# Kernel optimization log

Measured on AMD Instinct MI355X. Metric: run time of the kernel, lower is better.

Reference implementation:

```python
import jax, jax.numpy as jnp
import numpy as np

B, S, D, DM, H, DH, DF, L, T = 4096, 64, 256, 512, 4, 64, 512, 6, 20


def mish(x):
    return x * jnp.tanh(jax.nn.softplus(x))


def layernorm(x, eps=1e-5):
    mu = jnp.mean(x, axis=-1, keepdims=True)
    var = jnp.var(x, axis=-1, keepdims=True)
    return (x - mu) * jax.lax.rsqrt(var + eps)


def setup_inputs() -> dict:
    key = jax.random.key(0)
    ks = iter(jax.random.split(key, 32))
    w = lambda *shape: jax.random.normal(next(ks), shape, dtype=jnp.float32) * 0.02
    inp = {
        'x_t': jax.random.normal(next(ks), (B, S, D), dtype=jnp.float32),
        't': jax.random.randint(next(ks), (B,), 0, T + 1),
        'backbone_latent': jax.random.normal(next(ks), (B, S, DM), dtype=jnp.float32),
        # timestep embedding
        'emb': w(T + 1, D),
        'te_w1': w(D, 4 * D), 'te_b1': jnp.zeros((4 * D,), jnp.float32),
        'te_w2': w(4 * D, D), 'te_b2': jnp.zeros((D,), jnp.float32),
        # cond projection
        'cp_w1': w(DM, D), 'cp_b1': jnp.zeros((D,), jnp.float32),
        'cp_w2': w(D, D), 'cp_b2': jnp.zeros((D,), jnp.float32),
        # stacked per-layer DiT block params [L, ...]
        'adaln_w': w(L, D, 6 * D), 'adaln_b': jnp.zeros((L, 6 * D), jnp.float32),
        'qkv_w': w(L, D, 3 * D), 'qkv_b': jnp.zeros((L, 3 * D), jnp.float32),
        'op_w': w(L, D, D), 'op_b': jnp.zeros((L, D), jnp.float32),
        'ffn_w1': w(L, D, DF), 'ffn_b1': jnp.zeros((L, DF), jnp.float32),
        'ffn_w2': w(L, DF, D), 'ffn_b2': jnp.zeros((L, D), jnp.float32),
        # final adaLN + projection (random here for nontrivial test, zero-init in original)
        'fa_w': w(D, 2 * D), 'fa_b': jnp.zeros((2 * D,), jnp.float32),
        'fp_w': w(D, D), 'fp_b': jnp.zeros((D,), jnp.float32),
    }
    return inp


def _forward(x_t, t, backbone_latent, emb, te_w1, te_b1, te_w2, te_b2,
             cp_w1, cp_b1, cp_w2, cp_b2, adaln_w, adaln_b, qkv_w, qkv_b,
             op_w, op_b, ffn_w1, ffn_b1, ffn_w2, ffn_b2, fa_w, fa_b, fp_w, fp_b):
    # conditioning vector c: [B, D]
    te = emb[t]                                   # [B, D]
    te = mish(te @ te_w1 + te_b1) @ te_w2 + te_b2
    cond = jnp.mean(backbone_latent, axis=1)      # [B, DM]
    cond = mish(cond @ cp_w1 + cp_b1) @ cp_w2 + cp_b2
    c = te + cond
    mc = mish(c)

    x = x_t
    for l in range(L):
        mod = (mc @ adaln_w[l] + adaln_b[l])[:, None, :]   # [B, 1, 6D]
        sh1, sc1, g1, sh2, sc2, g2 = jnp.split(mod, 6, axis=-1)
        # attention sub-block
        h = layernorm(x) * (1.0 + sc1) + sh1
        qkv = (h @ qkv_w[l] + qkv_b[l]).reshape(B, S, 3, H, DH)
        q = qkv[:, :, 0].transpose(0, 2, 1, 3)   # [B, H, S, DH]
        k = qkv[:, :, 1].transpose(0, 2, 1, 3)
        v = qkv[:, :, 2].transpose(0, 2, 1, 3)
        attn = jax.nn.softmax(jnp.einsum('bhsd,bhtd->bhst', q, k) * DH ** -0.5, axis=-1)
        h = jnp.einsum('bhst,bhtd->bhsd', attn, v).transpose(0, 2, 1, 3).reshape(B, S, D)
        h = h @ op_w[l] + op_b[l]
        x = x + g1 * h
        # FFN sub-block
        h = layernorm(x) * (1.0 + sc2) + sh2
        h = mish(h @ ffn_w1[l] + ffn_b1[l]) @ ffn_w2[l] + ffn_b2[l]
        x = x + g2 * h

    mod = (mc @ fa_w + fa_b)[:, None, :]
    shift, scale = jnp.split(mod, 2, axis=-1)
    x = layernorm(x) * (1.0 + scale) + shift
    return x @ fp_w + fp_b


def reference(x_t, t, backbone_latent, emb, te_w1, te_b1, te_w2, te_b2,
              cp_w1, cp_b1, cp_w2, cp_b2, adaln_w, adaln_b, qkv_w, qkv_b,
              op_w, op_b, ffn_w1, ffn_b1, ffn_w2, ffn_b2, fa_w, fa_b, fp_w, fp_b):
    return _forward(x_t, t, backbone_latent, emb, te_w1, te_b1, te_w2, te_b2,
                    cp_w1, cp_b1, cp_w2, cp_b2, adaln_w, adaln_b, qkv_w, qkv_b,
                    op_w, op_b, ffn_w1, ffn_b1, ffn_w2, ffn_b2, fa_w, fa_b, fp_w, fp_b)
```

## Files before the change

### kernel.cpp

```cpp
#include <hip/hip_runtime.h>

typedef unsigned short u16;
typedef float f32x4 __attribute__((ext_vector_type(4)));
typedef __bf16 bf16x8 __attribute__((ext_vector_type(8)));

__device__ __forceinline__ u16 f2b(float f) {
  unsigned u = __builtin_bit_cast(unsigned, f);
  u += 0x7FFF + ((u >> 16) & 1);
  return (u16)(u >> 16);
}

__device__ __forceinline__ float mishf(float x) {
  float e = __expf(fminf(x, 20.f));
  float n = e * (e + 2.f);
  return x * __fdividef(n, n + 2.f);
}

__device__ __forceinline__ void gl_lds16(const void* g, void* l) {
  __builtin_amdgcn_global_load_lds((__attribute__((address_space(1))) void*)g,
                                   (__attribute__((address_space(3))) void*)l, 16, 0, 0);
}

__device__ __forceinline__ bf16x8 ldb8(const u16* p) {
  return __builtin_bit_cast(bf16x8, *(const uint4*)p);
}

__global__ __launch_bounds__(256)
void transpose_w(const float* __restrict__ in, u16* __restrict__ out, int K, int N) {
  __shared__ float tl[64][65];
  const long zoff = (long)blockIdx.z * K * N;
  in += zoff; out += zoff;
  const int n0 = blockIdx.x * 64, k0 = blockIdx.y * 64;
  const int c = threadIdx.x & 63, r0 = threadIdx.x >> 6;
#pragma unroll
  for (int i = 0; i < 16; ++i) {
    int r = i * 4 + r0;
    tl[r][c] = in[(long)(k0 + r) * N + n0 + c];
  }
  __syncthreads();
#pragma unroll
  for (int i = 0; i < 16; ++i) {
    int r = i * 4 + r0;
    out[(long)(n0 + r) * K + k0 + c] = f2b(tl[c][r]);
  }
}

__global__ __launch_bounds__(1024)
void te_table_kernel(const float* __restrict__ emb, const float* __restrict__ w1,
                     const float* __restrict__ b1, const float* __restrict__ w2,
                     const float* __restrict__ b2, float* __restrict__ table) {
  __shared__ float te[256];
  __shared__ float h1[1024];
  __shared__ float red[1024];
  const int tt = blockIdx.x, tid = threadIdx.x;
  if (tid < 256) te[tid] = emb[tt * 256 + tid];
  __syncthreads();
  float a = b1[tid];
#pragma unroll 8
  for (int k = 0; k < 256; ++k) a += te[k] * w1[k * 1024 + tid];
  h1[tid] = mishf(a);
  __syncthreads();
  const int j = tid & 255, kq = tid >> 8;
  float a2 = 0.f;
#pragma unroll 8
  for (int k = kq * 256; k < kq * 256 + 256; ++k) a2 += h1[k] * w2[k * 256 + j];
  red[tid] = a2;
  __syncthreads();
  if (tid < 256)
    table[tt * 256 + tid] = b2[tid] + red[tid] + red[tid + 256] + red[tid + 512] + red[tid + 768];
}

__global__ __launch_bounds__(256)
void cond_mean_kernel(const float* __restrict__ bb, u16* __restrict__ cond) {
  const int b = blockIdx.x, tid = threadIdx.x;
  const float* p = bb + (long)b * 64 * 512;
  for (int d = tid; d < 512; d += 256) {
    float s = 0.f;
#pragma unroll
    for (int t = 0; t < 64; ++t) s += p[t * 512 + d];
    cond[b * 512 + d] = f2b(s * (1.f / 64.f));
  }
}

__global__ __launch_bounds__(256)
void ln_mod(const float* __restrict__ x, const float* __restrict__ modb,
            int mstride, int shoff, int scoff, u16* __restrict__ out) {
  const int lane = threadIdx.x & 63;
  const long row = (long)blockIdx.x * 4 + (threadIdx.x >> 6);
  const float4 xv = *(const float4*)(x + row * 256 + lane * 4);
  float s1 = xv.x + xv.y + xv.z + xv.w;
  float s2 = xv.x * xv.x + xv.y * xv.y + xv.z * xv.z + xv.w * xv.w;
#pragma unroll
  for (int m = 1; m < 64; m <<= 1) { s1 += __shfl_xor(s1, m); s2 += __shfl_xor(s2, m); }
  const float mean = s1 * (1.f / 256.f);
  float var = s2 * (1.f / 256.f) - mean * mean;
  const float rstd = rsqrtf(fmaxf(var, 0.f) + 1e-5f);
  const long b = row >> 6;
  const float4 sc = *(const float4*)(modb + b * mstride + scoff + lane * 4);
  const float4 sh = *(const float4*)(modb + b * mstride + shoff + lane * 4);
  ushort4 o;
  o.x = f2b((xv.x - mean) * rstd * (1.f + sc.x) + sh.x);
  o.y = f2b((xv.y - mean) * rstd * (1.f + sc.y) + sh.y);
  o.z = f2b((xv.z - mean) * rstd * (1.f + sc.z) + sh.z);
  o.w = f2b((xv.w - mean) * rstd * (1.f + sc.w) + sh.w);
  *(ushort4*)(out + row * 256 + lane * 4) = o;
}

template <int EPI>
__global__ __launch_bounds__(256)
void gemm_bt(const u16* __restrict__ A, const u16* __restrict__ Bt,
             const float* __restrict__ bias, void* __restrict__ outp,
             const int* __restrict__ tvec, const float* __restrict__ tetab,
             int M, int N, int K) {
  __shared__ __align__(16) u16 As[2][128 * 64];
  __shared__ __align__(16) u16 Bs[2][128 * 64];
  const int tid = threadIdx.x;
  const int lane = tid & 63;
  const int wave = tid >> 6;
  const int wr = (wave >> 1) << 6;
  const int wc = (wave & 1) << 6;
  const long tm = (long)blockIdx.y * 128;
  const long tn = (long)blockIdx.x * 128;
  const u16* Ag = A + tm * K;
  const u16* Bg = Bt + tn * K;
  f32x4 acc[4][4] = {};
  const int kcb = lane >> 4;
  const int swz = lane & 7;
  const int NT = K >> 6;

  auto stage = [&](int t, int buf) {
    const int k0 = t << 6;
#pragma unroll
    for (int i = 0; i < 4; ++i) {
      int c = tid + (i << 8);
      int r = c >> 3;
      int sch = (c & 7) ^ (r & 7);
      gl_lds16(Ag + (long)r * K + k0 + (sch << 3), &As[buf][c << 3]);
    }
#pragma unroll
    for (int i = 0; i < 4; ++i) {
      int c = tid + (i << 8);
      int r = c >> 3;
      int sch = (c & 7) ^ (r & 7);
      gl_lds16(Bg + (long)r * K + k0 + (sch << 3), &Bs[buf][c << 3]);
    }
  };

  stage(0, 0);
  __syncthreads();
  int cur = 0;
  for (int t = 0; t < NT; ++t) {
    if (t + 1 < NT) stage(t + 1, cur ^ 1);
#pragma unroll
    for (int kt = 0; kt < 2; ++kt) {
      const int ko = ((kt * 4 + kcb) ^ swz) << 3;
      bf16x8 av[4], bv[4];
#pragma unroll
      for (int mt = 0; mt < 4; ++mt)
        av[mt] = ldb8(&As[cur][(wr + mt * 16 + (lane & 15)) * 64 + ko]);
#pragma unroll
      for (int nt = 0; nt < 4; ++nt)
        bv[nt] = ldb8(&Bs[cur][(wc + nt * 16 + (lane & 15)) * 64 + ko]);
#pragma unroll
      for (int mt = 0; mt < 4; ++mt)
#pragma unroll
        for (int nt = 0; nt < 4; ++nt)
          acc[mt][nt] = __builtin_amdgcn_mfma_f32_16x16x32_bf16(bv[nt], av[mt], acc[mt][nt], 0, 0, 0);
    }
    __syncthreads();
    cur ^= 1;
  }
  const int rl = lane & 15;
  const int c4 = (lane >> 4) << 2;
  f32x4 b4[4];
#pragma unroll
  for (int nt = 0; nt < 4; ++nt)
    b4[nt] = *(const f32x4*)(bias + (int)tn + wc + nt * 16 + c4);
#pragma unroll
  for (int mt = 0; mt < 4; ++mt) {
    const unsigned row = (unsigned)(tm + wr + mt * 16 + rl);
    const unsigned rb = row * (unsigned)N;
#pragma unroll
    for (int nt = 0; nt < 4; ++nt) {
      const unsigned col = (unsigned)tn + wc + nt * 16 + c4;
      f32x4 v = acc[mt][nt] + b4[nt];
      if constexpr (EPI == 0) {
        ushort4 o;
        o.x = f2b(v[0]); o.y = f2b(v[1]); o.z = f2b(v[2]); o.w = f2b(v[3]);
        *(ushort4*)((u16*)outp + rb + col) = o;
      } else if constexpr (EPI == 1) {
        ushort4 o;
        o.x = f2b(mishf(v[0])); o.y = f2b(mishf(v[1]));
        o.z = f2b(mishf(v[2])); o.w = f2b(mishf(v[3]));
        *(ushort4*)((u16*)outp + rb + col) = o;
      } else if constexpr (EPI == 3) {
        *(f32x4*)((float*)outp + rb + col) = v;
      } else {
        const f32x4 te = *(const f32x4*)(tetab + tvec[row] * 256 + col);
        ushort4 o;
        o.x = f2b(mishf(v[0] + te[0])); o.y = f2b(mishf(v[1] + te[1]));
        o.z = f2b(mishf(v[2] + te[2])); o.w = f2b(mishf(v[3] + te[3]));
        *(ushort4*)((u16*)outp + rb + col) = o;
      }
    }
  }
}

__global__ __launch_bounds__(256)
void gemm_ln(const u16* __restrict__ A, const u16* __restrict__ Bt,
             const float* __restrict__ bias, const float* __restrict__ xin,
             const float* __restrict__ gptr,
             const float* __restrict__ lnsh, const float* __restrict__ lnsc, int lnstride,
             float* __restrict__ xout, u16* __restrict__ hout, int K) {
  __shared__ __align__(16) u16 As[2][64 * 64];
  __shared__ __align__(16) u16 Bs[2][256 * 64];
  const int tid = threadIdx.x, lane = tid & 63, wave = tid >> 6;
  const int wr = wave * 16;
  const long tm = (long)blockIdx.x * 64;
  const u16* Ag = A + tm * K;
  f32x4 acc[16] = {};
  const int kcb = lane >> 4, swz = lane & 7;
  const int NT = K >> 6;

  auto stage = [&](int t, int buf) {
    const int k0 = t << 6;
#pragma unroll
    for (int i = 0; i < 2; ++i) {
      int c = tid + (i << 8);
      int r = c >> 3;
      int sch = (c & 7) ^ (r & 7);
      gl_lds16(Ag + (long)r * K + k0 + (sch << 3), &As[buf][c << 3]);
    }
#pragma unroll
    for (int i = 0; i < 8; ++i) {
      int c = tid + (i << 8);
      int r = c >> 3;
      int sch = (c & 7) ^ (r & 7);
      gl_lds16(Bt + (long)r * K + k0 + (sch << 3), &Bs[buf][c << 3]);
    }
  };

  stage(0, 0);
  __syncthreads();
  int cur = 0;
  for (int t = 0; t < NT; ++t) {
    if (t + 1 < NT) stage(t + 1, cur ^ 1);
#pragma unroll
    for (int kt = 0; kt < 2; ++kt) {
      const int ko = ((kt * 4 + kcb) ^ swz) << 3;
      bf16x8 av = ldb8(&As[cur][(wr + (lane & 15)) * 64 + ko]);
#pragma unroll
      for (int nt = 0; nt < 16; ++nt) {
        bf16x8 bv = ldb8(&Bs[cur][(nt * 16 + (lane & 15)) * 64 + ko]);
        acc[nt] = __builtin_amdgcn_mfma_f32_16x16x32_bf16(bv, av, acc[nt], 0, 0, 0);
      }
    }
    __syncthreads();
    cur ^= 1;
  }
  const int rl = lane & 15;
  const int c4 = (lane >> 4) << 2;
  const long row = tm + wr + rl;
  const long b = blockIdx.x;
  float s1 = 0.f, s2 = 0.f;
#pragma unroll
  for (int nt = 0; nt < 16; ++nt) {
    const int col = nt * 16 + c4;
    const f32x4 b4 = *(const f32x4*)(bias + col);
    const f32x4 g4 = *(const f32x4*)(gptr + b * 1536 + col);
    const f32x4 x = *(const f32x4*)(xin + row * 256 + col);
    f32x4 xn = x + g4 * (acc[nt] + b4);
    acc[nt] = xn;
    s1 += xn[0] + xn[1] + xn[2] + xn[3];
    s2 += xn[0] * xn[0] + xn[1] * xn[1] + xn[2] * xn[2] + xn[3] * xn[3];
  }
  s1 += __shfl_xor(s1, 16); s1 += __shfl_xor(s1, 32);
  s2 += __shfl_xor(s2, 16); s2 += __shfl_xor(s2, 32);
  const float mean = s1 * (1.f / 256.f);
  const float var = s2 * (1.f / 256.f) - mean * mean;
  const float rstd = rsqrtf(fmaxf(var, 0.f) + 1e-5f);
#pragma unroll
  for (int nt = 0; nt < 16; ++nt) {
    const int col = nt * 16 + c4;
    const f32x4 sc4 = *(const f32x4*)(lnsc + b * lnstride + col);
    const f32x4 sh4 = *(const f32x4*)(lnsh + b * lnstride + col);
    *(f32x4*)(xout + row * 256 + col) = acc[nt];
    f32x4 h = (acc[nt] - mean) * rstd * (1.f + sc4) + sh4;
    ushort4 o;
    o.x = f2b(h[0]); o.y = f2b(h[1]); o.z = f2b(h[2]); o.w = f2b(h[3]);
    *(ushort4*)(hout + row * 256 + col) = o;
  }
}

__global__ __launch_bounds__(128)
void attn_kernel(const u16* __restrict__ qkv, u16* __restrict__ out) {
  __shared__ __align__(16) u16 vt_s[2][64 * 72];
  __shared__ __align__(16) u16 p_s[2][64 * 72];
  const int lane = threadIdx.x & 63;
  const int wave = threadIdx.x >> 6;
  const long b = blockIdx.x >> 1;
  const int h = ((blockIdx.x & 1) << 1) | wave;
  u16* vt = vt_s[wave];
  u16* pl = p_s[wave];
  const u16* base = qkv + b * (64 * 768);
#pragma unroll
  for (int it = 0; it < 8; ++it) {
    int chunk = it * 64 + lane;
    int t = chunk >> 3, dhb = (chunk & 7) << 3;
    union { uint4 u; u16 s[8]; } uv;
    uv.u = *(const uint4*)(base + t * 768 + 512 + h * 64 + dhb);
#pragma unroll
    for (int j = 0; j < 8; ++j) vt[(dhb + j) * 72 + t] = uv.s[j];
  }
  const u16* qb = base + h * 64;
  const u16* kb = base + 256 + h * 64;
  f32x4 sacc[4][4] = {};
#pragma unroll
  for (int kt = 0; kt < 2; ++kt) {
    bf16x8 qa[4], kv[4];
#pragma unroll
    for (int mt = 0; mt < 4; ++mt)
      qa[mt] = ldb8(qb + ((lane & 15) + mt * 16) * 768 + kt * 32 + ((lane >> 4) << 3));
#pragma unroll
    for (int nt = 0; nt < 4; ++nt)
      kv[nt] = ldb8(kb + ((lane & 15) + nt * 16) * 768 + kt * 32 + ((lane >> 4) << 3));
#pragma unroll
    for (int mt = 0; mt < 4; ++mt)
#pragma unroll
      for (int nt = 0; nt < 4; ++nt)
        sacc[mt][nt] = __builtin_amdgcn_mfma_f32_16x16x32_bf16(qa[mt], kv[nt], sacc[mt][nt], 0, 0, 0);
  }
  const float scale = 0.125f;
#pragma unroll
  for (int mt = 0; mt < 4; ++mt) {
#pragma unroll
    for (int r = 0; r < 4; ++r) {
      float mx = fmaxf(fmaxf(sacc[mt][0][r], sacc[mt][1][r]), fmaxf(sacc[mt][2][r], sacc[mt][3][r]));
#pragma unroll
      for (int m = 1; m <= 8; m <<= 1) mx = fmaxf(mx, __shfl_xor(mx, m));
      float p[4];
      float sum = 0.f;
#pragma unroll
      for (int nt = 0; nt < 4; ++nt) { p[nt] = __expf((sacc[mt][nt][r] - mx) * scale); sum += p[nt]; }
#pragma unroll
      for (int m = 1; m <= 8; m <<= 1) sum += __shfl_xor(sum, m);
      const float rinv = 1.f / sum;
      const int s = mt * 16 + ((lane >> 4) << 2) + r;
#pragma unroll
      for (int nt = 0; nt < 4; ++nt) pl[s * 72 + nt * 16 + (lane & 15)] = f2b(p[nt] * rinv);
    }
  }
  __syncthreads();
  f32x4 oacc[4][4] = {};
#pragma unroll
  for (int kt = 0; kt < 2; ++kt) {
    bf16x8 pa[4], vv[4];
#pragma unroll
    for (int mt = 0; mt < 4; ++mt)
      pa[mt] = ldb8(pl + ((lane & 15) + mt * 16) * 72 + kt * 32 + ((lane >> 4) << 3));
#pragma unroll
    for (int nt = 0; nt < 4; ++nt)
      vv[nt] = ldb8(vt + ((lane & 15) + nt * 16) * 72 + kt * 32 + ((lane >> 4) << 3));
#pragma unroll
    for (int mt = 0; mt < 4; ++mt)
#pragma unroll
      for (int nt = 0; nt < 4; ++nt)
        oacc[mt][nt] = __builtin_amdgcn_mfma_f32_16x16x32_bf16(vv[nt], pa[mt], oacc[mt][nt], 0, 0, 0);
  }
  u16* ob = out + b * (64 * 256) + h * 64;
#pragma unroll
  for (int mt = 0; mt < 4; ++mt)
#pragma unroll
    for (int nt = 0; nt < 4; ++nt) {
      const int s = mt * 16 + (lane & 15);
      const int d4 = nt * 16 + ((lane >> 4) << 2);
      ushort4 o;
      o.x = f2b(oacc[mt][nt][0]); o.y = f2b(oacc[mt][nt][1]);
      o.z = f2b(oacc[mt][nt][2]); o.w = f2b(oacc[mt][nt][3]);
      *(ushort4*)(ob + s * 256 + d4) = o;
    }
}

extern "C" void kernel_launch(void* const* d_in, const int* in_sizes, int n_in,
                              void* d_out, int out_size, void* d_ws, size_t ws_size,
                              hipStream_t stream) {
  (void)in_sizes; (void)n_in; (void)out_size; (void)ws_size;
  const int B = 4096, L = 6;
  const long BSr = (long)B * 64;

  const float* x_t = (const float*)d_in[0];
  const int* tvec = (const int*)d_in[1];
  const float* backbone = (const float*)d_in[2];
  const float* emb = (const float*)d_in[3];
  const float* te_w1 = (const float*)d_in[4];
  const float* te_b1 = (const float*)d_in[5];
  const float* te_w2 = (const float*)d_in[6];
  const float* te_b2 = (const float*)d_in[7];
  const float* cp_w1 = (const float*)d_in[8];
  const float* cp_b1 = (const float*)d_in[9];
  const float* cp_w2 = (const float*)d_in[10];
  const float* cp_b2 = (const float*)d_in[11];
  const float* adaln_w = (const float*)d_in[12];
  const float* adaln_b = (const float*)d_in[13];
  const float* qkv_w = (const float*)d_in[14];
  const float* qkv_b = (const float*)d_in[15];
  const float* op_w = (const float*)d_in[16];
  const float* op_b = (const float*)d_in[17];
  const float* ffn_w1 = (const float*)d_in[18];
  const float* ffn_b1 = (const float*)d_in[19];
  const float* ffn_w2 = (const float*)d_in[20];
  const float* ffn_b2 = (const float*)d_in[21];
  const float* fa_w = (const float*)d_in[22];
  const float* fa_b = (const float*)d_in[23];
  const float* fp_w = (const float*)d_in[24];
  const float* fp_b = (const float*)d_in[25];

  char* w = (char*)d_ws;
  auto alloc = [&](size_t bytes) { char* p = w; w += (bytes + 255) & ~(size_t)255; return p; };
  u16* WT_cp1 = (u16*)alloc(256L * 512 * 2);
  u16* WT_cp2 = (u16*)alloc(256L * 256 * 2);
  u16* WT_adaln = (u16*)alloc(6L * 1536 * 256 * 2);
  u16* WT_qkv = (u16*)alloc(6L * 768 * 256 * 2);
  u16* WT_op = (u16*)alloc(6L * 256 * 256 * 2);
  u16* WT_f1 = (u16*)alloc(6L * 512 * 256 * 2);
  u16* WT_f2 = (u16*)alloc(6L * 256 * 512 * 2);
  u16* WT_fa = (u16*)alloc(512L * 256 * 2);
  u16* WT_fp = (u16*)alloc(256L * 256 * 2);
  float* te_tab = (float*)alloc(21L * 256 * 4);
  u16* cond = (u16*)alloc(4096L * 512 * 2);
  u16* c1 = (u16*)alloc(4096L * 256 * 2);
  u16* mc = (u16*)alloc(4096L * 256 * 2);
  float* modb6 = (float*)alloc(6L * 4096 * 1536 * 4);
  float* famod = (float*)alloc(4096L * 512 * 4);
  u16* hbuf = (u16*)alloc(BSr * 256 * 2);
  u16* qkvbuf = (u16*)alloc(BSr * 768 * 2);
  float* xbuf = (float*)d_out;

  transpose_w<<<dim3(4, 8, 1), 256, 0, stream>>>(cp_w1, WT_cp1, 512, 256);
  transpose_w<<<dim3(4, 4, 1), 256, 0, stream>>>(cp_w2, WT_cp2, 256, 256);
  transpose_w<<<dim3(24, 4, 6), 256, 0, stream>>>(adaln_w, WT_adaln, 256, 1536);
  transpose_w<<<dim3(12, 4, 6), 256, 0, stream>>>(qkv_w, WT_qkv, 256, 768);
  transpose_w<<<dim3(4, 4, 6), 256, 0, stream>>>(op_w, WT_op, 256, 256);
  transpose_w<<<dim3(8, 4, 6), 256, 0, stream>>>(ffn_w1, WT_f1, 256, 512);
  transpose_w<<<dim3(4, 8, 6), 256, 0, stream>>>(ffn_w2, WT_f2, 512, 256);
  transpose_w<<<dim3(8, 4, 1), 256, 0, stream>>>(fa_w, WT_fa, 256, 512);
  transpose_w<<<dim3(4, 4, 1), 256, 0, stream>>>(fp_w, WT_fp, 256, 256);

  te_table_kernel<<<21, 1024, 0, stream>>>(emb, te_w1, te_b1, te_w2, te_b2, te_tab);
  cond_mean_kernel<<<4096, 256, 0, stream>>>(backbone, cond);

  gemm_bt<1><<<dim3(2, 32), 256, 0, stream>>>(cond, WT_cp1, cp_b1, c1, nullptr, nullptr, 4096, 256, 512);
  gemm_bt<4><<<dim3(2, 32), 256, 0, stream>>>(c1, WT_cp2, cp_b2, mc, tvec, te_tab, 4096, 256, 256);
  gemm_bt<3><<<dim3(4, 32), 256, 0, stream>>>(mc, WT_fa, fa_b, famod, nullptr, nullptr, 4096, 512, 256);
  for (int l = 0; l < L; ++l)
    gemm_bt<3><<<dim3(12, 32), 256, 0, stream>>>(mc, WT_adaln + (long)l * 1536 * 256, adaln_b + l * 1536,
                                                 modb6 + (long)l * 4096 * 1536, nullptr, nullptr, 4096, 1536, 256);

  ln_mod<<<BSr / 4, 256, 0, stream>>>(x_t, modb6, 1536, 0, 256, hbuf);

  for (int l = 0; l < L; ++l) {
    const float* mb = modb6 + (long)l * 4096 * 1536;
    gemm_bt<0><<<dim3(6, BSr / 128), 256, 0, stream>>>(hbuf, WT_qkv + (long)l * 768 * 256, qkv_b + l * 768,
                                                       qkvbuf, nullptr, nullptr, (int)BSr, 768, 256);
    attn_kernel<<<B * 2, 128, 0, stream>>>(qkvbuf, hbuf);
    gemm_ln<<<BSr / 64, 256, 0, stream>>>(hbuf, WT_op + (long)l * 256 * 256, op_b + l * 256,
                                          (l == 0) ? x_t : xbuf, mb + 512,
                                          mb + 768, mb + 1024, 1536, xbuf, hbuf, 256);
    gemm_bt<1><<<dim3(4, BSr / 128), 256, 0, stream>>>(hbuf, WT_f1 + (long)l * 512 * 256, ffn_b1 + l * 512,
                                                       qkvbuf, nullptr, nullptr, (int)BSr, 512, 256);
    const float* nsh = (l < 5) ? (modb6 + (long)(l + 1) * 4096 * 1536) : famod;
    const float* nsc = (l < 5) ? (modb6 + (long)(l + 1) * 4096 * 1536 + 256) : (famod + 256);
    const int nstride = (l < 5) ? 1536 : 512;
    gemm_ln<<<BSr / 64, 256, 0, stream>>>(qkvbuf, WT_f2 + (long)l * 256 * 512, ffn_b2 + l * 256,
                                          xbuf, mb + 1280, nsh, nsc, nstride, xbuf, hbuf, 512);
  }
  gemm_bt<3><<<dim3(2, BSr / 128), 256, 0, stream>>>(hbuf, WT_fp, fp_b, d_out, nullptr, nullptr, (int)BSr, 256, 256);
}
```

Measured before the change: 7.059 ms.

## Retile gemm_ln waves to 64x64 subtiles with cross-wave LayerNorm reduction

Each wave in the fused GEMM+residual+LayerNorm kernel now computes a 64-row by 64-column subtile instead of 16 rows by all 256 columns. This cuts the shared-memory B-fragment reads per MFMA, since each wave now loads 4 A and 4 B fragments for 16 MFMAs instead of 1 A and 16 B. Because a row is now split across waves, row sums go through shared memory with an extra barrier. The residual, gate and bias loads are also issued before the main loop so they overlap the first stage, and K becomes a template parameter. The prefetched values raise register pressure.

```diff
diff --git a/kernel.cpp b/kernel.cpp
--- a/kernel.cpp
+++ b/kernel.cpp
@@ -206,20 +206,22 @@
   }
 }
 
+template <int K>
 __global__ __launch_bounds__(256)
 void gemm_ln(const u16* __restrict__ A, const u16* __restrict__ Bt,
              const float* __restrict__ bias, const float* __restrict__ xin,
              const float* __restrict__ gptr,
              const float* __restrict__ lnsh, const float* __restrict__ lnsc, int lnstride,
-             float* __restrict__ xout, u16* __restrict__ hout, int K) {
+             float* __restrict__ xout, u16* __restrict__ hout) {
   __shared__ __align__(16) u16 As[2][64 * 64];
   __shared__ __align__(16) u16 Bs[2][256 * 64];
   const int tid = threadIdx.x, lane = tid & 63, wave = tid >> 6;
-  const int wr = wave * 16;
+  const int wc = wave << 6;
   const long tm = (long)blockIdx.x * 64;
   const u16* Ag = A + tm * K;
-  f32x4 acc[16] = {};
-  const int kcb = lane >> 4, swz = lane & 7;
+  const int rl = lane & 15;
+  const int c4 = (lane >> 4) << 2;
+  const int swz = lane & 7;
   const int NT = K >> 6;
 
   auto stage = [&](int t, int buf) {
@@ -241,54 +243,94 @@
   };
 
   stage(0, 0);
-  __syncthreads();
+  const long b = blockIdx.x;
+  f32x4 xr[4][4], g4[4], b4[4];
+#pragma unroll
+  for (int nt = 0; nt < 4; ++nt) {
+    const int col = wc + nt * 16 + c4;
+    b4[nt] = *(const f32x4*)(bias + col);
+    g4[nt] = *(const f32x4*)(gptr + b * 1536 + col);
+#pragma unroll
+    for (int mt = 0; mt < 4; ++mt)
+      xr[mt][nt] = *(const f32x4*)(xin + (tm + mt * 16 + rl) * 256 + col);
+  }
+  __syncthreads();
+
+  f32x4 acc[4][4] = {};
   int cur = 0;
   for (int t = 0; t < NT; ++t) {
     if (t + 1 < NT) stage(t + 1, cur ^ 1);
 #pragma unroll
     for (int kt = 0; kt < 2; ++kt) {
-      const int ko = ((kt * 4 + kcb) ^ swz) << 3;
-      bf16x8 av = ldb8(&As[cur][(wr + (lane & 15)) * 64 + ko]);
-#pragma unroll
-      for (int nt = 0; nt < 16; ++nt) {
-        bf16x8 bv = ldb8(&Bs[cur][(nt * 16 + (lane & 15)) * 64 + ko]);
-        acc[nt] = __builtin_amdgcn_mfma_f32_16x16x32_bf16(bv, av, acc[nt], 0, 0, 0);
-      }
+      const int ko = ((kt * 4 + (lane >> 4)) ^ swz) << 3;
+      bf16x8 av[4], bv[4];
+#pragma unroll
+      for (int mt = 0; mt < 4; ++mt)
+        av[mt] = ldb8(&As[cur][(mt * 16 + rl) * 64 + ko]);
+#pragma unroll
+      for (int nt = 0; nt < 4; ++nt)
+        bv[nt] = ldb8(&Bs[cur][(wc + nt * 16 + rl) * 64 + ko]);
+#pragma unroll
+      for (int mt = 0; mt < 4; ++mt)
+#pragma unroll
+        for (int nt = 0; nt < 4; ++nt)
+          acc[mt][nt] = __builtin_amdgcn_mfma_f32_16x16x32_bf16(bv[nt], av[mt], acc[mt][nt], 0, 0, 0);
     }
     __syncthreads();
     cur ^= 1;
   }
-  const int rl = lane & 15;
-  const int c4 = (lane >> 4) << 2;
-  const long row = tm + wr + rl;
-  const long b = blockIdx.x;
-  float s1 = 0.f, s2 = 0.f;
-#pragma unroll
-  for (int nt = 0; nt < 16; ++nt) {
-    const int col = nt * 16 + c4;
-    const f32x4 b4 = *(const f32x4*)(bias + col);
-    const f32x4 g4 = *(const f32x4*)(gptr + b * 1536 + col);
-    const f32x4 x = *(const f32x4*)(xin + row * 256 + col);
-    f32x4 xn = x + g4 * (acc[nt] + b4);
-    acc[nt] = xn;
-    s1 += xn[0] + xn[1] + xn[2] + xn[3];
-    s2 += xn[0] * xn[0] + xn[1] * xn[1] + xn[2] * xn[2] + xn[3] * xn[3];
-  }
-  s1 += __shfl_xor(s1, 16); s1 += __shfl_xor(s1, 32);
-  s2 += __shfl_xor(s2, 16); s2 += __shfl_xor(s2, 32);
-  const float mean = s1 * (1.f / 256.f);
-  const float var = s2 * (1.f / 256.f) - mean * mean;
-  const float rstd = rsqrtf(fmaxf(var, 0.f) + 1e-5f);
-#pragma unroll
-  for (int nt = 0; nt < 16; ++nt) {
-    const int col = nt * 16 + c4;
+
+  float s1[4] = {}, s2[4] = {};
+#pragma unroll
+  for (int mt = 0; mt < 4; ++mt)
+#pragma unroll
+    for (int nt = 0; nt < 4; ++nt) {
+      f32x4 xn = xr[mt][nt] + g4[nt] * (acc[mt][nt] + b4[nt]);
+      acc[mt][nt] = xn;
+      s1[mt] += xn[0] + xn[1] + xn[2] + xn[3];
+      s2[mt] += xn[0] * xn[0] + xn[1] * xn[1] + xn[2] * xn[2] + xn[3] * xn[3];
+    }
+#pragma unroll
+  for (int mt = 0; mt < 4; ++mt) {
+    s1[mt] += __shfl_xor(s1[mt], 16); s1[mt] += __shfl_xor(s1[mt], 32);
+    s2[mt] += __shfl_xor(s2[mt], 16); s2[mt] += __shfl_xor(s2[mt], 32);
+  }
+  float* st = (float*)&As[0][0];
+  if (lane < 16) {
+#pragma unroll
+    for (int mt = 0; mt < 4; ++mt) {
+      st[wave * 128 + mt * 16 + lane] = s1[mt];
+      st[wave * 128 + 64 + mt * 16 + lane] = s2[mt];
+    }
+  }
+  __syncthreads();
+  float mean[4], rstd[4];
+#pragma unroll
+  for (int mt = 0; mt < 4; ++mt) {
+    float a = 0.f, q = 0.f;
+#pragma unroll
+    for (int w2 = 0; w2 < 4; ++w2) {
+      a += st[w2 * 128 + mt * 16 + rl];
+      q += st[w2 * 128 + 64 + mt * 16 + rl];
+    }
+    mean[mt] = a * (1.f / 256.f);
+    float var = q * (1.f / 256.f) - mean[mt] * mean[mt];
+    rstd[mt] = rsqrtf(fmaxf(var, 0.f) + 1e-5f);
+  }
+#pragma unroll
+  for (int nt = 0; nt < 4; ++nt) {
+    const int col = wc + nt * 16 + c4;
     const f32x4 sc4 = *(const f32x4*)(lnsc + b * lnstride + col);
     const f32x4 sh4 = *(const f32x4*)(lnsh + b * lnstride + col);
-    *(f32x4*)(xout + row * 256 + col) = acc[nt];
-    f32x4 h = (acc[nt] - mean) * rstd * (1.f + sc4) + sh4;
-    ushort4 o;
-    o.x = f2b(h[0]); o.y = f2b(h[1]); o.z = f2b(h[2]); o.w = f2b(h[3]);
-    *(ushort4*)(hout + row * 256 + col) = o;
+#pragma unroll
+    for (int mt = 0; mt < 4; ++mt) {
+      const long row = tm + mt * 16 + rl;
+      *(f32x4*)(xout + row * 256 + col) = acc[mt][nt];
+      f32x4 h = (acc[mt][nt] - mean[mt]) * rstd[mt] * (1.f + sc4) + sh4;
+      ushort4 o;
+      o.x = f2b(h[0]); o.y = f2b(h[1]); o.z = f2b(h[2]); o.w = f2b(h[3]);
+      *(ushort4*)(hout + row * 256 + col) = o;
+    }
   }
 }
 
@@ -463,16 +505,16 @@
     gemm_bt<0><<<dim3(6, BSr / 128), 256, 0, stream>>>(hbuf, WT_qkv + (long)l * 768 * 256, qkv_b + l * 768,
                                                        qkvbuf, nullptr, nullptr, (int)BSr, 768, 256);
     attn_kernel<<<B * 2, 128, 0, stream>>>(qkvbuf, hbuf);
-    gemm_ln<<<BSr / 64, 256, 0, stream>>>(hbuf, WT_op + (long)l * 256 * 256, op_b + l * 256,
-                                          (l == 0) ? x_t : xbuf, mb + 512,
-                                          mb + 768, mb + 1024, 1536, xbuf, hbuf, 256);
+    gemm_ln<256><<<BSr / 64, 256, 0, stream>>>(hbuf, WT_op + (long)l * 256 * 256, op_b + l * 256,
+                                               (l == 0) ? x_t : xbuf, mb + 512,
+                                               mb + 768, mb + 1024, 1536, xbuf, hbuf);
     gemm_bt<1><<<dim3(4, BSr / 128), 256, 0, stream>>>(hbuf, WT_f1 + (long)l * 512 * 256, ffn_b1 + l * 512,
                                                        qkvbuf, nullptr, nullptr, (int)BSr, 512, 256);
     const float* nsh = (l < 5) ? (modb6 + (long)(l + 1) * 4096 * 1536) : famod;
     const float* nsc = (l < 5) ? (modb6 + (long)(l + 1) * 4096 * 1536 + 256) : (famod + 256);
     const int nstride = (l < 5) ? 1536 : 512;
-    gemm_ln<<<BSr / 64, 256, 0, stream>>>(qkvbuf, WT_f2 + (long)l * 256 * 512, ffn_b2 + l * 256,
-                                          xbuf, mb + 1280, nsh, nsc, nstride, xbuf, hbuf, 512);
+    gemm_ln<512><<<BSr / 64, 256, 0, stream>>>(qkvbuf, WT_f2 + (long)l * 256 * 512, ffn_b2 + l * 256,
+                                               xbuf, mb + 1280, nsh, nsc, nstride, xbuf, hbuf);
   }
   gemm_bt<3><<<dim3(2, BSr / 128), 256, 0, stream>>>(hbuf, WT_fp, fp_b, d_out, nullptr, nullptr, (int)BSr, 256, 256);
 }
```

New measurement: 7.134 ms. No clear change (+1.1%).
